# Kernel tuning notes

Hardware: AMD Instinct MI355X
Metric: run time of the kernel (lower is better)

The kernel has to match this reference:

```python
import jax, jax.numpy as jnp
import numpy as np

EMB_DIM = 1024
N_HEADS = 16
HEAD_DIM = EMB_DIM // N_HEADS


def setup_inputs() -> dict:
    key = jax.random.key(0)
    ks = jax.random.split(key, 6)
    B, S, D = 2, 2048, EMB_DIM
    scale = 1.0 / np.sqrt(D)
    return {
        "in_data": jax.random.normal(ks[0], (B, S, D), dtype=jnp.float32),
        "Wq": jax.random.normal(ks[1], (D, D), dtype=jnp.float32) * scale,
        "Wk": jax.random.normal(ks[2], (D, D), dtype=jnp.float32) * scale,
        "Wv": jax.random.normal(ks[3], (D, D), dtype=jnp.float32) * scale,
        "Wo": jax.random.normal(ks[4], (D, D), dtype=jnp.float32) * scale,
        "bo": jax.random.normal(ks[5], (D,), dtype=jnp.float32) * 0.01,
    }


def reference(in_data, Wq, Wk, Wv, Wo, bo):
    B, S, D = in_data.shape
    H, Hd = N_HEADS, HEAD_DIM
    # Linear projections (qvbias=False): torch Linear is x @ W.T
    q = in_data @ Wq.T
    k = in_data @ Wk.T
    v = in_data @ Wv.T
    # split heads -> (B, H, S, Hd)
    q = q.reshape(B, S, H, Hd).transpose(0, 2, 1, 3)
    k = k.reshape(B, S, H, Hd).transpose(0, 2, 1, 3)
    v = v.reshape(B, S, H, Hd).transpose(0, 2, 1, 3)
    # scores (B, H, S, S), causal mask applied BEFORE scaling (as in source)
    scores = jnp.einsum("bhqd,bhkd->bhqk", q, k)
    causal = jnp.triu(jnp.ones((S, S), dtype=bool), k=1)
    scores = jnp.where(causal, -jnp.inf, scores)
    scores = scores / jnp.sqrt(jnp.asarray(Hd, dtype=scores.dtype))
    attn = jax.nn.softmax(scores, axis=-1)
    # dropout with drop_rate=0.0 -> identity
    ctx = jnp.einsum("bhqk,bhkd->bhqd", attn, v)
    ctx = ctx.transpose(0, 2, 1, 3).reshape(B, S, D)
    out = ctx @ Wo.T + bo
    return out
```

## Files before the change

kernel.cpp:

```cpp
#include <hip/hip_runtime.h>

typedef _Float16 f16;
typedef _Float16 f16x2 __attribute__((ext_vector_type(2)));
typedef _Float16 f16x4 __attribute__((ext_vector_type(4)));
typedef _Float16 f16x8 __attribute__((ext_vector_type(8)));
typedef float f32x4 __attribute__((ext_vector_type(4)));
typedef int i32x4 __attribute__((ext_vector_type(4)));

#define MFMA(a, b, c) __builtin_amdgcn_mfma_f32_16x16x32_f16((a), (b), (c), 0, 0, 0)

typedef __attribute__((address_space(1))) const void gvoid;
typedef __attribute__((address_space(3))) void lvoid;

__device__ __forceinline__ void gload16(const void* g, void* l) {
    __builtin_amdgcn_global_load_lds((gvoid*)g, (lvoid*)l, 16, 0, 0);
}

__global__ void cast_all(const float* __restrict__ x,
                         const float* __restrict__ w0, const float* __restrict__ w1,
                         const float* __restrict__ w2, const float* __restrict__ w3,
                         f16* __restrict__ xb, f16* __restrict__ wb,
                         float* __restrict__ out0) {
    const int NX = 4096 * 1024;
    const int blk = blockIdx.x;
    if (blk >= 8192) {
        int idx = (blk - 8192) * 1024 + threadIdx.x * 4;
        float4 z = {0.f, 0.f, 0.f, 0.f};
        *(float4*)(out0 + idx) = z;
        return;
    }
    int i = (blk * 256 + threadIdx.x) * 4;
    if (i < NX) {
        float4 v = *(const float4*)(x + i);
        f16x4 o = {(f16)v.x, (f16)v.y, (f16)v.z, (f16)v.w};
        *(f16x4*)(xb + i) = o;
    } else {
        int j = i - NX;
        const float* s = (j < (1 << 20)) ? w0 : (j < (2 << 20)) ? w1
                       : (j < (3 << 20)) ? w2 : w3;
        int loc = j & ((1 << 20) - 1);
        float4 v = *(const float4*)(s + loc);
        f16x4 o = {(f16)v.x, (f16)v.y, (f16)v.z, (f16)v.w};
        *(f16x4*)(wb + j) = o;
    }
}

__global__ void gemm_qkv(const f16* __restrict__ A, const f16* __restrict__ W,
                         f16* __restrict__ Qo, f16* __restrict__ Ko,
                         f16* __restrict__ VTo) {
    __shared__ __align__(16) f16 As[128 * 64];
    __shared__ __align__(16) f16 Bs[128 * 64];
    const int tid = threadIdx.x;
    const int lane = tid & 63, wid = tid >> 6;
    const int lo = lane & 15, hi = lane >> 4;
    const int wr = wid >> 1, wc = wid & 1;
    const int m0 = blockIdx.x * 128, n0 = blockIdx.y * 128;
    const int z = blockIdx.z;
    const char* Ab = (const char*)A;
    const char* Bb = (const char*)(W + (size_t)z * (1024 * 1024));

    f32x4 acc[4][4];
#pragma unroll
    for (int i = 0; i < 4; ++i)
#pragma unroll
        for (int j = 0; j < 4; ++j) acc[i][j] = (f32x4){0.f, 0.f, 0.f, 0.f};

    for (int kt = 0; kt < 16; ++kt) {
        const int kb = kt * 128;
#pragma unroll
        for (int rr = 0; rr < 4; ++rr) {
            int o = rr * 4096 + tid * 16;
            int row = o >> 7, colB = o & 127;
            gload16(Ab + (size_t)(m0 + row) * 2048 + kb + colB, (char*)As + o);
            gload16(Bb + (size_t)(n0 + row) * 2048 + kb + colB, (char*)Bs + o);
        }
        __syncthreads();
#pragma unroll
        for (int kc = 0; kc < 2; ++kc) {
            f16x8 af[4], bf[4];
#pragma unroll
            for (int f = 0; f < 4; ++f)
                af[f] = *(const f16x8*)(As + (wr * 64 + f * 16 + lo) * 64 + kc * 32 + hi * 8);
#pragma unroll
            for (int f = 0; f < 4; ++f)
                bf[f] = *(const f16x8*)(Bs + (wc * 64 + f * 16 + lo) * 64 + kc * 32 + hi * 8);
#pragma unroll
            for (int i = 0; i < 4; ++i)
#pragma unroll
                for (int j = 0; j < 4; ++j) acc[i][j] = MFMA(af[i], bf[j], acc[i][j]);
        }
        __syncthreads();
    }

    const int mbase = m0 + wr * 64 + hi * 4;
    const int nbase = n0 + wc * 64 + lo;
    if (z == 0) {
#pragma unroll
        for (int i = 0; i < 4; ++i)
#pragma unroll
            for (int j = 0; j < 4; ++j)
#pragma unroll
                for (int r = 0; r < 4; ++r)
                    Qo[(size_t)(mbase + i * 16 + r) * 1024 + nbase + j * 16] =
                        (f16)(acc[i][j][r] * 0.18033688f);
    } else if (z == 1) {
#pragma unroll
        for (int i = 0; i < 4; ++i)
#pragma unroll
            for (int j = 0; j < 4; ++j)
#pragma unroll
                for (int r = 0; r < 4; ++r)
                    Ko[(size_t)(mbase + i * 16 + r) * 1024 + nbase + j * 16] =
                        (f16)acc[i][j][r];
    } else {
#pragma unroll
        for (int i = 0; i < 4; ++i)
#pragma unroll
            for (int j = 0; j < 4; ++j)
#pragma unroll
                for (int r = 0; r < 4; ++r) {
                    const int m = mbase + i * 16 + r, n = nbase + j * 16;
                    VTo[(size_t)((m >> 11) * 1024 + n) * 2048 + (m & 2047)] =
                        (f16)acc[i][j][r];
                }
    }
}

__global__ __launch_bounds__(256) void attn(const f16* __restrict__ Q,
                                            const f16* __restrict__ K,
                                            const f16* __restrict__ VT,
                                            f16* __restrict__ CTX) {
    __shared__ __align__(16) f16 K0[64 * 64];
    __shared__ __align__(16) f16 K1[64 * 64];
    __shared__ __align__(16) f16 K2[64 * 64];
    __shared__ __align__(16) f16 K3[64 * 64];
    __shared__ __align__(16) f16 V0[64 * 64];
    __shared__ __align__(16) f16 V1[64 * 64];
    __shared__ __align__(16) f16 V2[64 * 64];
    __shared__ __align__(16) f16 V3[64 * 64];
    const int tid = threadIdx.x;
    const int lane = tid & 63, w = tid >> 6;
    const int lo = lane & 15, hi = lane >> 4;
    const int bh = blockIdx.x;
    const int qt = 31 - blockIdx.y;
    const int b = bh >> 4, h = bh & 15;
    const int qw0 = qt * 64 + w * 16;
    const int qglob = qw0 + lo;
    const int nt = qt + 1;

    const f16* qrow = Q + (size_t)(b * 2048 + qw0 + lo) * 1024 + h * 64 + hi * 8;
    const f16x8 qa0 = *(const f16x8*)(qrow);
    const f16x8 qa1 = *(const f16x8*)(qrow + 32);

    f32x4 ctx[4];
#pragma unroll
    for (int d = 0; d < 4; ++d) ctx[d] = (f32x4){0.f, 0.f, 0.f, 0.f};
    float mrun = -3e38f, lsum = 0.f;

    const int idx0 = (2 * (hi & 1)) * 16 + lo;
    const int idx1 = idx0 + 16;

    const char* Kb = (const char*)K;
    const char* Vb = (const char*)VT;

    auto stage = [&](f16* Kd, f16* Vd, int t) {
        const int kv0 = t * 64;
#pragma unroll
        for (int rr = 0; rr < 2; ++rr) {
            int o = rr * 4096 + tid * 16;
            int row = o >> 7;
            int colB = (o & 127) ^ ((row & 7) << 4);
            gload16(Kb + (size_t)(b * 2048 + kv0 + row) * 2048 + h * 128 + colB,
                    (char*)Kd + o);
            gload16(Vb + (size_t)(b * 1024 + h * 64 + row) * 4096 + (size_t)kv0 * 2 + colB,
                    (char*)Vd + o);
        }
    };

    auto compute = [&](const f16* Klb, const f16* Vlb, int t) {
        f32x4 s4[4];
        __builtin_amdgcn_s_setprio(1);
#pragma unroll
        for (int fj = 0; fj < 4; ++fj) {
            f32x4 a = (f32x4){0.f, 0.f, 0.f, 0.f};
            const int kv = fj * 16 + lo;
#pragma unroll
            for (int kc = 0; kc < 2; ++kc) {
                const int cb = (kc * 64 + hi * 16) ^ ((kv & 7) << 4);
                f16x8 kf = *(const f16x8*)((const char*)Klb + kv * 128 + cb);
                a = MFMA(kf, kc ? qa1 : qa0, a);
            }
            s4[fj] = a;
        }
        __builtin_amdgcn_s_setprio(0);

        float pv[16];
        if (t == qt) {
#pragma unroll
            for (int fj = 0; fj < 4; ++fj)
#pragma unroll
                for (int r = 0; r < 4; ++r) {
                    const int kvg = t * 64 + fj * 16 + hi * 4 + r;
                    pv[fj * 4 + r] = (kvg > qglob) ? -1e38f : s4[fj][r];
                }
        } else {
#pragma unroll
            for (int fj = 0; fj < 4; ++fj)
#pragma unroll
                for (int r = 0; r < 4; ++r) pv[fj * 4 + r] = s4[fj][r];
        }

        float tm[8];
#pragma unroll
        for (int i = 0; i < 8; ++i) tm[i] = fmaxf(pv[i], pv[i + 8]);
#pragma unroll
        for (int i = 0; i < 4; ++i) tm[i] = fmaxf(tm[i], tm[i + 4]);
        const float mxl = fmaxf(fmaxf(tm[0], tm[1]), fmaxf(tm[2], tm[3]));

        if (__any(mxl > mrun + 8.0f)) {
            float mxg = fmaxf(mxl, __shfl_xor(mxl, 16));
            mxg = fmaxf(mxg, __shfl_xor(mxg, 32));
            const float mnew = fmaxf(mrun, mxg);
            const float corr = __builtin_amdgcn_exp2f(mrun - mnew);
            mrun = mnew;
            lsum *= corr;
#pragma unroll
            for (int d = 0; d < 4; ++d) {
                ctx[d][0] *= corr; ctx[d][1] *= corr;
                ctx[d][2] *= corr; ctx[d][3] *= corr;
            }
        }

#pragma unroll
        for (int i = 0; i < 16; ++i) pv[i] = __builtin_amdgcn_exp2f(pv[i] - mrun);
        float ts[8];
#pragma unroll
        for (int i = 0; i < 8; ++i) ts[i] = pv[i] + pv[i + 8];
#pragma unroll
        for (int i = 0; i < 4; ++i) ts[i] = ts[i] + ts[i + 4];
        lsum += (ts[0] + ts[1]) + (ts[2] + ts[3]);

        int ph[4][2];
#pragma unroll
        for (int fj = 0; fj < 4; ++fj)
#pragma unroll
            for (int r2 = 0; r2 < 2; ++r2) {
                f16x2 hpair = {(f16)pv[fj * 4 + 2 * r2], (f16)pv[fj * 4 + 2 * r2 + 1]};
                ph[fj][r2] = __builtin_bit_cast(int, hpair);
            }

        f16x8 pb[2];
#pragma unroll
        for (int kc = 0; kc < 2; ++kc) {
            i32x4 dw;
#pragma unroll
            for (int j2 = 0; j2 < 4; ++j2) {
                const int idx = (j2 < 2) ? idx0 : idx1;
                int vA = __shfl(ph[2 * kc][j2 & 1], idx);
                int vB = __shfl(ph[2 * kc + 1][j2 & 1], idx);
                dw[j2] = (hi & 2) ? vB : vA;
            }
            pb[kc] = __builtin_bit_cast(f16x8, dw);
        }

        __builtin_amdgcn_s_setprio(1);
#pragma unroll
        for (int df = 0; df < 4; ++df) {
            const int d = df * 16 + lo;
#pragma unroll
            for (int kc = 0; kc < 2; ++kc) {
                const int cb = (kc * 64 + hi * 16) ^ ((d & 7) << 4);
                f16x8 vf = *(const f16x8*)((const char*)Vlb + d * 128 + cb);
                ctx[df] = MFMA(vf, pb[kc], ctx[df]);
            }
        }
        __builtin_amdgcn_s_setprio(0);
    };

    stage(&K0[0], &V0[0], 0);
    if (nt > 1) stage(&K1[0], &V1[0], 1);
    for (int p = 0; p < nt; p += 2) {
        __syncthreads();
        if (((p >> 1) & 1) == 0) {
            if (p + 2 < nt) stage(&K2[0], &V2[0], p + 2);
            if (p + 3 < nt) stage(&K3[0], &V3[0], p + 3);
            compute(&K0[0], &V0[0], p);
            if (p + 1 < nt) compute(&K1[0], &V1[0], p + 1);
        } else {
            if (p + 2 < nt) stage(&K0[0], &V0[0], p + 2);
            if (p + 3 < nt) stage(&K1[0], &V1[0], p + 3);
            compute(&K2[0], &V2[0], p);
            if (p + 1 < nt) compute(&K3[0], &V3[0], p + 1);
        }
    }

    float lt = lsum + __shfl_xor(lsum, 16);
    lt += __shfl_xor(lt, 32);
    const float inv = 1.0f / lt;
#pragma unroll
    for (int df = 0; df < 4; ++df) {
        f16x4 o = {(f16)(ctx[df][0] * inv), (f16)(ctx[df][1] * inv),
                   (f16)(ctx[df][2] * inv), (f16)(ctx[df][3] * inv)};
        *(f16x4*)(CTX + (size_t)(b * 2048 + qw0 + lo) * 1024 + h * 64 + df * 16 + hi * 4) = o;
    }
}

__global__ void gemm_proj(const f16* __restrict__ A, const f16* __restrict__ Bw,
                          float* __restrict__ Co, const float* __restrict__ bias) {
    __shared__ __align__(16) f16 As[128 * 64];
    __shared__ __align__(16) f16 Bs[128 * 64];
    const int tid = threadIdx.x;
    const int lane = tid & 63, wid = tid >> 6;
    const int lo = lane & 15, hi = lane >> 4;
    const int wr = wid >> 1, wc = wid & 1;
    const int m0 = blockIdx.x * 128, n0 = blockIdx.y * 128;
    const int z = blockIdx.z;
    const char* Ab = (const char*)A;
    const char* Bb = (const char*)Bw;

    f32x4 acc[4][4];
#pragma unroll
    for (int i = 0; i < 4; ++i)
#pragma unroll
        for (int j = 0; j < 4; ++j) acc[i][j] = (f32x4){0.f, 0.f, 0.f, 0.f};

    for (int kt = z * 4; kt < z * 4 + 4; ++kt) {
        const int kb = kt * 128;
#pragma unroll
        for (int rr = 0; rr < 4; ++rr) {
            int o = rr * 4096 + tid * 16;
            int row = o >> 7, colB = o & 127;
            gload16(Ab + (size_t)(m0 + row) * 2048 + kb + colB, (char*)As + o);
            gload16(Bb + (size_t)(n0 + row) * 2048 + kb + colB, (char*)Bs + o);
        }
        __syncthreads();
#pragma unroll
        for (int kc = 0; kc < 2; ++kc) {
            f16x8 af[4], bf[4];
#pragma unroll
            for (int f = 0; f < 4; ++f)
                af[f] = *(const f16x8*)(As + (wr * 64 + f * 16 + lo) * 64 + kc * 32 + hi * 8);
#pragma unroll
            for (int f = 0; f < 4; ++f)
                bf[f] = *(const f16x8*)(Bs + (wc * 64 + f * 16 + lo) * 64 + kc * 32 + hi * 8);
#pragma unroll
            for (int i = 0; i < 4; ++i)
#pragma unroll
                for (int j = 0; j < 4; ++j) acc[i][j] = MFMA(af[i], bf[j], acc[i][j]);
        }
        __syncthreads();
    }

    const int mbase = m0 + wr * 64 + hi * 4;
    const int nbase = n0 + wc * 64 + lo;
#pragma unroll
    for (int j = 0; j < 4; ++j) {
        const float bj = (z == 0) ? bias[nbase + j * 16] : 0.f;
#pragma unroll
        for (int i = 0; i < 4; ++i)
#pragma unroll
            for (int r = 0; r < 4; ++r)
                atomicAdd(&Co[(size_t)(mbase + i * 16 + r) * 1024 + nbase + j * 16],
                          acc[i][j][r] + bj);
    }
}

extern "C" void kernel_launch(void* const* d_in, const int* in_sizes, int n_in,
                              void* d_out, int out_size, void* d_ws, size_t ws_size,
                              hipStream_t stream) {
    const float* x = (const float*)d_in[0];
    const float* wq = (const float*)d_in[1];
    const float* wk = (const float*)d_in[2];
    const float* wv = (const float*)d_in[3];
    const float* wo = (const float*)d_in[4];
    const float* bo = (const float*)d_in[5];

    const size_t M1 = 1024 * 1024;
    f16* VT = (f16*)d_ws;
    f16* Wh = VT + 4 * M1;
    f16* QKV = Wh + 4 * M1;
    f16* Xb = QKV + 8 * M1;
    f16* Q = QKV;
    f16* K = QKV + 4 * M1;
    f16* CTX = QKV + 8 * M1;
    float* out = (float*)d_out;

    cast_all<<<dim3(12288), dim3(256), 0, stream>>>(x, wq, wk, wv, wo, Xb, Wh, out);
    gemm_qkv<<<dim3(32, 8, 3), dim3(256), 0, stream>>>(Xb, Wh, Q, K, VT);
    attn<<<dim3(32, 32), dim3(256), 0, stream>>>(Q, K, VT, CTX);
    gemm_proj<<<dim3(32, 8, 4), dim3(256), 0, stream>>>(CTX, Wh + 3 * M1, out, bo);
}
```

Measured before the change: 229.1 us.

## Widen GEMM K-tiles with swizzled LDS, drop split-K atomics, shrink attention buffering

Both GEMMs now stage 256-wide K tiles into XOR-swizzled shared memory, which halves the number of barrier rounds and is meant to avoid LDS bank conflicts. The output projection drops its 4-way split-K with atomicAdd and writes directly with the bias added, so the zeroing pass in the cast kernel is removed. The attention kernel goes from four-deep to two-deep K/V buffering, which cuts shared memory use and may raise occupancy but hides less load latency. The projection GEMM now launches a quarter as many blocks, which reduces parallelism on a large GPU.

```diff
diff --git a/kernel.cpp b/kernel.cpp
--- a/kernel.cpp
+++ b/kernel.cpp
@@ -19,17 +19,9 @@
 __global__ void cast_all(const float* __restrict__ x,
                          const float* __restrict__ w0, const float* __restrict__ w1,
                          const float* __restrict__ w2, const float* __restrict__ w3,
-                         f16* __restrict__ xb, f16* __restrict__ wb,
-                         float* __restrict__ out0) {
+                         f16* __restrict__ xb, f16* __restrict__ wb) {
     const int NX = 4096 * 1024;
-    const int blk = blockIdx.x;
-    if (blk >= 8192) {
-        int idx = (blk - 8192) * 1024 + threadIdx.x * 4;
-        float4 z = {0.f, 0.f, 0.f, 0.f};
-        *(float4*)(out0 + idx) = z;
-        return;
-    }
-    int i = (blk * 256 + threadIdx.x) * 4;
+    int i = (blockIdx.x * 256 + threadIdx.x) * 4;
     if (i < NX) {
         float4 v = *(const float4*)(x + i);
         f16x4 o = {(f16)v.x, (f16)v.y, (f16)v.z, (f16)v.w};
@@ -48,8 +40,8 @@
 __global__ void gemm_qkv(const f16* __restrict__ A, const f16* __restrict__ W,
                          f16* __restrict__ Qo, f16* __restrict__ Ko,
                          f16* __restrict__ VTo) {
-    __shared__ __align__(16) f16 As[128 * 64];
-    __shared__ __align__(16) f16 Bs[128 * 64];
+    __shared__ __align__(16) f16 As[128 * 128];
+    __shared__ __align__(16) f16 Bs[128 * 128];
     const int tid = threadIdx.x;
     const int lane = tid & 63, wid = tid >> 6;
     const int lo = lane & 15, hi = lane >> 4;
@@ -65,25 +57,32 @@
 #pragma unroll
         for (int j = 0; j < 4; ++j) acc[i][j] = (f32x4){0.f, 0.f, 0.f, 0.f};
 
-    for (int kt = 0; kt < 16; ++kt) {
-        const int kb = kt * 128;
-#pragma unroll
-        for (int rr = 0; rr < 4; ++rr) {
+    for (int kt = 0; kt < 8; ++kt) {
+        const int kb = kt * 256;
+#pragma unroll
+        for (int rr = 0; rr < 8; ++rr) {
             int o = rr * 4096 + tid * 16;
-            int row = o >> 7, colB = o & 127;
+            int row = o >> 8;
+            int colB = (o & 255) ^ ((row & 7) << 4);
             gload16(Ab + (size_t)(m0 + row) * 2048 + kb + colB, (char*)As + o);
             gload16(Bb + (size_t)(n0 + row) * 2048 + kb + colB, (char*)Bs + o);
         }
         __syncthreads();
 #pragma unroll
-        for (int kc = 0; kc < 2; ++kc) {
+        for (int kc = 0; kc < 4; ++kc) {
             f16x8 af[4], bf[4];
 #pragma unroll
-            for (int f = 0; f < 4; ++f)
-                af[f] = *(const f16x8*)(As + (wr * 64 + f * 16 + lo) * 64 + kc * 32 + hi * 8);
-#pragma unroll
-            for (int f = 0; f < 4; ++f)
-                bf[f] = *(const f16x8*)(Bs + (wc * 64 + f * 16 + lo) * 64 + kc * 32 + hi * 8);
+            for (int f = 0; f < 4; ++f) {
+                const int row = wr * 64 + f * 16 + lo;
+                const int cb = (kc * 64 + hi * 16) ^ ((row & 7) << 4);
+                af[f] = *(const f16x8*)((const char*)As + row * 256 + cb);
+            }
+#pragma unroll
+            for (int f = 0; f < 4; ++f) {
+                const int row = wc * 64 + f * 16 + lo;
+                const int cb = (kc * 64 + hi * 16) ^ ((row & 7) << 4);
+                bf[f] = *(const f16x8*)((const char*)Bs + row * 256 + cb);
+            }
 #pragma unroll
             for (int i = 0; i < 4; ++i)
 #pragma unroll
@@ -132,12 +131,8 @@
                                             f16* __restrict__ CTX) {
     __shared__ __align__(16) f16 K0[64 * 64];
     __shared__ __align__(16) f16 K1[64 * 64];
-    __shared__ __align__(16) f16 K2[64 * 64];
-    __shared__ __align__(16) f16 K3[64 * 64];
     __shared__ __align__(16) f16 V0[64 * 64];
     __shared__ __align__(16) f16 V1[64 * 64];
-    __shared__ __align__(16) f16 V2[64 * 64];
-    __shared__ __align__(16) f16 V3[64 * 64];
     const int tid = threadIdx.x;
     const int lane = tid & 63, w = tid >> 6;
     const int lo = lane & 15, hi = lane >> 4;
@@ -146,7 +141,6 @@
     const int b = bh >> 4, h = bh & 15;
     const int qw0 = qt * 64 + w * 16;
     const int qglob = qw0 + lo;
-    const int nt = qt + 1;
 
     const f16* qrow = Q + (size_t)(b * 2048 + qw0 + lo) * 1024 + h * 64 + hi * 8;
     const f16x8 qa0 = *(const f16x8*)(qrow);
@@ -278,19 +272,14 @@
     };
 
     stage(&K0[0], &V0[0], 0);
-    if (nt > 1) stage(&K1[0], &V1[0], 1);
-    for (int p = 0; p < nt; p += 2) {
-        __syncthreads();
-        if (((p >> 1) & 1) == 0) {
-            if (p + 2 < nt) stage(&K2[0], &V2[0], p + 2);
-            if (p + 3 < nt) stage(&K3[0], &V3[0], p + 3);
-            compute(&K0[0], &V0[0], p);
-            if (p + 1 < nt) compute(&K1[0], &V1[0], p + 1);
+    for (int t = 0; t <= qt; ++t) {
+        __syncthreads();
+        if ((t & 1) == 0) {
+            if (t < qt) stage(&K1[0], &V1[0], t + 1);
+            compute(&K0[0], &V0[0], t);
         } else {
-            if (p + 2 < nt) stage(&K0[0], &V0[0], p + 2);
-            if (p + 3 < nt) stage(&K1[0], &V1[0], p + 3);
-            compute(&K2[0], &V2[0], p);
-            if (p + 1 < nt) compute(&K3[0], &V3[0], p + 1);
+            if (t < qt) stage(&K0[0], &V0[0], t + 1);
+            compute(&K1[0], &V1[0], t);
         }
     }
 
@@ -307,14 +296,13 @@
 
 __global__ void gemm_proj(const f16* __restrict__ A, const f16* __restrict__ Bw,
                           float* __restrict__ Co, const float* __restrict__ bias) {
-    __shared__ __align__(16) f16 As[128 * 64];
-    __shared__ __align__(16) f16 Bs[128 * 64];
+    __shared__ __align__(16) f16 As[128 * 128];
+    __shared__ __align__(16) f16 Bs[128 * 128];
     const int tid = threadIdx.x;
     const int lane = tid & 63, wid = tid >> 6;
     const int lo = lane & 15, hi = lane >> 4;
     const int wr = wid >> 1, wc = wid & 1;
     const int m0 = blockIdx.x * 128, n0 = blockIdx.y * 128;
-    const int z = blockIdx.z;
     const char* Ab = (const char*)A;
     const char* Bb = (const char*)Bw;
 
@@ -324,25 +312,32 @@
 #pragma unroll
         for (int j = 0; j < 4; ++j) acc[i][j] = (f32x4){0.f, 0.f, 0.f, 0.f};
 
-    for (int kt = z * 4; kt < z * 4 + 4; ++kt) {
-        const int kb = kt * 128;
-#pragma unroll
-        for (int rr = 0; rr < 4; ++rr) {
+    for (int kt = 0; kt < 8; ++kt) {
+        const int kb = kt * 256;
+#pragma unroll
+        for (int rr = 0; rr < 8; ++rr) {
             int o = rr * 4096 + tid * 16;
-            int row = o >> 7, colB = o & 127;
+            int row = o >> 8;
+            int colB = (o & 255) ^ ((row & 7) << 4);
             gload16(Ab + (size_t)(m0 + row) * 2048 + kb + colB, (char*)As + o);
             gload16(Bb + (size_t)(n0 + row) * 2048 + kb + colB, (char*)Bs + o);
         }
         __syncthreads();
 #pragma unroll
-        for (int kc = 0; kc < 2; ++kc) {
+        for (int kc = 0; kc < 4; ++kc) {
             f16x8 af[4], bf[4];
 #pragma unroll
-            for (int f = 0; f < 4; ++f)
-                af[f] = *(const f16x8*)(As + (wr * 64 + f * 16 + lo) * 64 + kc * 32 + hi * 8);
-#pragma unroll
-            for (int f = 0; f < 4; ++f)
-                bf[f] = *(const f16x8*)(Bs + (wc * 64 + f * 16 + lo) * 64 + kc * 32 + hi * 8);
+            for (int f = 0; f < 4; ++f) {
+                const int row = wr * 64 + f * 16 + lo;
+                const int cb = (kc * 64 + hi * 16) ^ ((row & 7) << 4);
+                af[f] = *(const f16x8*)((const char*)As + row * 256 + cb);
+            }
+#pragma unroll
+            for (int f = 0; f < 4; ++f) {
+                const int row = wc * 64 + f * 16 + lo;
+                const int cb = (kc * 64 + hi * 16) ^ ((row & 7) << 4);
+                bf[f] = *(const f16x8*)((const char*)Bs + row * 256 + cb);
+            }
 #pragma unroll
             for (int i = 0; i < 4; ++i)
 #pragma unroll
@@ -355,13 +350,13 @@
     const int nbase = n0 + wc * 64 + lo;
 #pragma unroll
     for (int j = 0; j < 4; ++j) {
-        const float bj = (z == 0) ? bias[nbase + j * 16] : 0.f;
+        const float bj = bias[nbase + j * 16];
 #pragma unroll
         for (int i = 0; i < 4; ++i)
 #pragma unroll
             for (int r = 0; r < 4; ++r)
-                atomicAdd(&Co[(size_t)(mbase + i * 16 + r) * 1024 + nbase + j * 16],
-                          acc[i][j][r] + bj);
+                Co[(size_t)(mbase + i * 16 + r) * 1024 + nbase + j * 16] =
+                    acc[i][j][r] + bj;
     }
 }
 
@@ -385,8 +380,8 @@
     f16* CTX = QKV + 8 * M1;
     float* out = (float*)d_out;
 
-    cast_all<<<dim3(12288), dim3(256), 0, stream>>>(x, wq, wk, wv, wo, Xb, Wh, out);
+    cast_all<<<dim3(8192), dim3(256), 0, stream>>>(x, wq, wk, wv, wo, Xb, Wh);
     gemm_qkv<<<dim3(32, 8, 3), dim3(256), 0, stream>>>(Xb, Wh, Q, K, VT);
     attn<<<dim3(32, 32), dim3(256), 0, stream>>>(Q, K, VT, CTX);
-    gemm_proj<<<dim3(32, 8, 4), dim3(256), 0, stream>>>(CTX, Wh + 3 * M1, out, bo);
-}
+    gemm_proj<<<dim3(32, 8), dim3(256), 0, stream>>>(CTX, Wh + 3 * M1, out, bo);
+}
```

Measured after the change: 188.3 us. 1.22x faster.
